# Kernel tuning notes

Hardware: AMD Instinct MI355X
Metric: run time of the kernel (lower is better)

The kernel has to match this reference:

```python
import jax, jax.numpy as jnp
import numpy as np


def setup_inputs() -> dict:
    key = jax.random.key(0)
    k1, k2, k3 = jax.random.split(key, 3)
    B, D, L = 32768, 1024, 2
    return {
        "x": jax.random.normal(k1, (B, D), dtype=jnp.float32),
        "local_angles": jax.random.normal(k2, (L, D), dtype=jnp.float32),
        "ent_angles": jax.random.normal(k3, (L, D // 2), dtype=jnp.float32),
    }


def _local_layer(out, angles):
    # Sequential chain of Givens rotations on column pairs (i, (i+1)%D).
    # Each step uses the already-updated columns, exactly like the torch loop
    # (out = out @ R.T  ==  rotate columns i and j of out).
    D = out.shape[1]
    idx = jnp.arange(D)

    def body(o, inp):
        i, theta = inp
        j = (i + 1) % D
        c, s = jnp.cos(theta), jnp.sin(theta)
        ci = jnp.take(o, i, axis=1)  # [B]
        cj = jnp.take(o, j, axis=1)  # [B]
        o = o.at[:, i].set(c * ci - s * cj)
        o = o.at[:, j].set(s * ci + c * cj)
        return o, None

    out, _ = jax.lax.scan(body, out, (idx, angles))
    return out


def _ent_layer(out, angles):
    # Entangler rotations act on disjoint pairs (2k, 2k+1) -> fully vectorized.
    B, D = out.shape
    p = out.reshape(B, D // 2, 2)
    c, s = jnp.cos(angles), jnp.sin(angles)  # [D//2]
    x0, x1 = p[..., 0], p[..., 1]
    return jnp.stack([c * x0 - s * x1, s * x0 + c * x1], axis=-1).reshape(B, D)


def reference(x, local_angles, ent_angles):
    out = x
    num_layers = local_angles.shape[0]
    for l in range(num_layers):
        out = _local_layer(out, local_angles[l])
        out = _ent_layer(out, ent_angles[l])
    return out
```

## Files before the change

kernel.cpp:

```cpp
#include <hip/hip_runtime.h>

#define D_DIM    1024
#define PER_LANE 16
#define NLAYER   2
#define NPAIR    8
#define WPB      4

__device__ __forceinline__ int swz(int c) { return c ^ ((c >> 3) & 7); }

__global__ void angles_kernel(const float* __restrict__ la,
                              const float* __restrict__ ea,
                              float* __restrict__ tab) {
    int t  = blockIdx.x * blockDim.x + threadIdx.x;
    int nt = gridDim.x * blockDim.x;
    for (int i = t; i < NLAYER * D_DIM; i += nt) {
        float s, c; sincosf(la[i], &s, &c);
        tab[i] = c; tab[2048 + i] = s;
    }
    for (int i = t; i < NLAYER * (D_DIM / 2); i += nt) {
        float s, c; sincosf(ea[i], &s, &c);
        tab[4096 + i] = c; tab[5120 + i] = s;
    }
}

__global__ __launch_bounds__(256) void qent_kernel(
        const float* __restrict__ x,
        const float* __restrict__ tab,
        float* __restrict__ out, int B)
{
    const int lane  = threadIdx.x & 63;
    const int wid   = threadIdx.x >> 6;
    const int gwave = blockIdx.x * WPB + wid;
    const int nwave = gridDim.x * WPB;

    __shared__ float4 tb[WPB][2][256];
    __shared__ float  lds_ce[NLAYER][NPAIR][64];
    __shared__ float  lds_se[NLAYER][NPAIR][64];

    for (int t = threadIdx.x; t < NLAYER * 512; t += 256) {
        int L = t >> 9, p = t & 511;
        int m = p >> 6, ln = p & 63;
        lds_ce[L][m][ln] = tab[4096 + L * 512 + ln * 8 + m];
        lds_se[L][m][ln] = tab[5120 + L * 512 + ln * 8 + m];
    }
    __syncthreads();

    float cl[NLAYER][PER_LANE], sl[NLAYER][PER_LANE];
    #pragma unroll
    for (int L = 0; L < NLAYER; ++L) {
        const float4* cp = reinterpret_cast<const float4*>(tab + L * D_DIM + lane * PER_LANE);
        const float4* sp = reinterpret_cast<const float4*>(tab + 2048 + L * D_DIM + lane * PER_LANE);
        #pragma unroll
        for (int q = 0; q < 4; ++q) {
            float4 c4 = cp[q], s4 = sp[q];
            cl[L][4*q+0] = c4.x; cl[L][4*q+1] = c4.y; cl[L][4*q+2] = c4.z; cl[L][4*q+3] = c4.w;
            sl[L][4*q+0] = s4.x; sl[L][4*q+1] = s4.y; sl[L][4*q+2] = s4.z; sl[L][4*q+3] = s4.w;
        }
    }

    const int l2 = lane ^ (lane >> 3);
    auto stage = [&](int b, int row) {
        const float* src = x + (size_t)row * D_DIM;
        #pragma unroll
        for (int q = 0; q < 4; ++q) {
            __builtin_amdgcn_global_load_lds(
                (const __attribute__((address_space(1))) void*)(src + q * 256 + l2 * 4),
                (__attribute__((address_space(3))) void*)&tb[wid][b][q * 64],
                16, 0, 0);
        }
    };

    stage(0, gwave);

    int it = 0;
    for (int row = gwave; row < B; row += nwave, ++it) {
        const int cur  = it & 1;
        const int nrow = row + nwave;

        if (nrow < B) {
            stage(cur ^ 1, nrow);
            asm volatile("s_waitcnt vmcnt(4)" ::: "memory");
        } else {
            asm volatile("s_waitcnt vmcnt(0)" ::: "memory");
        }

        float v[PER_LANE];
        #pragma unroll
        for (int r = 0; r < 4; ++r) {
            float4 t = tb[wid][cur][swz(4 * lane + r)];
            v[4*r+0] = t.x; v[4*r+1] = t.y; v[4*r+2] = t.z; v[4*r+3] = t.w;
        }

        #pragma unroll
        for (int L = 0; L < NLAYER; ++L) {
            float vnf = __shfl_down(v[0], 1);

            float A = 1.f, Bv = 0.f;
            #pragma unroll
            for (int k = 0; k < PER_LANE; ++k) {
                float vn = (k < PER_LANE - 1) ? v[k + 1] : vnf;
                Bv = sl[L][k] * Bv + cl[L][k] * vn;
                A  = sl[L][k] * A;
            }

            float Ai = A, Bi = Bv;
            #pragma unroll
            for (int dd = 1; dd < 64; dd <<= 1) {
                float Au = __shfl_up(Ai, dd);
                float Bu = __shfl_up(Bi, dd);
                if (lane >= dd) {
                    Bi = Ai * Bu + Bi;
                    Ai = Ai * Au;
                }
            }
            float Ax  = __shfl_up(Ai, 1);
            float Bx  = __shfl_up(Bi, 1);
            float v0b = __shfl(v[0], 0);
            float u   = (lane == 0) ? v[0] : (Ax * v0b + Bx);

            #pragma unroll
            for (int k = 0; k < PER_LANE - 1; ++k) {
                float vn = v[k + 1];
                float f  = cl[L][k] * u - sl[L][k] * vn;
                u        = sl[L][k] * u + cl[L][k] * vn;
                v[k] = f;
            }
            float a0   = __shfl(v[0], 0);
            float vn15 = (lane == 63) ? a0 : vnf;
            float f15  = cl[L][PER_LANE-1] * u - sl[L][PER_LANE-1] * vn15;
            float un   = sl[L][PER_LANE-1] * u + cl[L][PER_LANE-1] * vn15;
            v[PER_LANE-1] = f15;
            float f0new = __shfl(un, 63);
            if (lane == 0) v[0] = f0new;

            #pragma unroll
            for (int m = 0; m < NPAIR; ++m) {
                float cem = lds_ce[L][m][lane];
                float sem = lds_se[L][m][lane];
                float x0 = v[2*m], x1 = v[2*m+1];
                v[2*m]   = cem * x0 - sem * x1;
                v[2*m+1] = sem * x0 + cem * x1;
            }
        }

        #pragma unroll
        for (int r = 0; r < 4; ++r) {
            float4 t;
            t.x = v[4*r+0]; t.y = v[4*r+1]; t.z = v[4*r+2]; t.w = v[4*r+3];
            tb[wid][cur][swz(4 * lane + r)] = t;
        }
        float4* op = reinterpret_cast<float4*>(out + (size_t)row * D_DIM);
        #pragma unroll
        for (int q = 0; q < 4; ++q) {
            float4 t = tb[wid][cur][swz(q * 64 + lane)];
            op[q * 64 + lane] = t;
        }
    }
}

extern "C" void kernel_launch(void* const* d_in, const int* in_sizes, int n_in,
                              void* d_out, int out_size, void* d_ws, size_t ws_size,
                              hipStream_t stream) {
    const float* x  = (const float*)d_in[0];
    const float* la = (const float*)d_in[1];
    const float* ea = (const float*)d_in[2];
    float* out = (float*)d_out;
    float* tab = (float*)d_ws;
    int B = in_sizes[0] / D_DIM;

    angles_kernel<<<8, 256, 0, stream>>>(la, ea, tab);
    qent_kernel<<<1024, 256, 0, stream>>>(x, tab, out, B);
}
```

Baseline: 62.14 us.

## Use DPP row shifts for wave scan and scalar readlanes for broadcasts

Replaces the ds_bpermute-based shuffle-up prefix scan of affine (A,B) pairs with DPP row_shr and row_bcast moves, which keep the data movement inside VALU instructions and avoid LDS permute traffic. Lane-0 and lane-63 broadcasts now use readfirstlane and readlane instead of shuffles. The entangler cos/sin values are packed into float2 so each pair needs one LDS read. The wait count is relaxed to vmcnt(8) after the first iteration, but this also lets the previous row's output stores stay in flight and relies on the exact instruction ordering for correctness.

```diff
diff --git a/kernel.cpp b/kernel.cpp
--- a/kernel.cpp
+++ b/kernel.cpp
@@ -7,6 +7,12 @@
 #define WPB      4
 
 __device__ __forceinline__ int swz(int c) { return c ^ ((c >> 3) & 7); }
+
+template<int CTRL, int RMASK>
+__device__ __forceinline__ float dpp_mov(float src, float oldv) {
+    return __int_as_float(__builtin_amdgcn_update_dpp(
+        __float_as_int(oldv), __float_as_int(src), CTRL, RMASK, 0xF, false));
+}
 
 __global__ void angles_kernel(const float* __restrict__ la,
                               const float* __restrict__ ea,
@@ -34,14 +40,15 @@
     const int nwave = gridDim.x * WPB;
 
     __shared__ float4 tb[WPB][2][256];
-    __shared__ float  lds_ce[NLAYER][NPAIR][64];
-    __shared__ float  lds_se[NLAYER][NPAIR][64];
+    __shared__ float2 lds_ces[NLAYER][NPAIR][64];
 
     for (int t = threadIdx.x; t < NLAYER * 512; t += 256) {
         int L = t >> 9, p = t & 511;
         int m = p >> 6, ln = p & 63;
-        lds_ce[L][m][ln] = tab[4096 + L * 512 + ln * 8 + m];
-        lds_se[L][m][ln] = tab[5120 + L * 512 + ln * 8 + m];
+        float2 cs;
+        cs.x = tab[4096 + L * 512 + ln * 8 + m];
+        cs.y = tab[5120 + L * 512 + ln * 8 + m];
+        lds_ces[L][m][ln] = cs;
     }
     __syncthreads();
 
@@ -79,7 +86,8 @@
 
         if (nrow < B) {
             stage(cur ^ 1, nrow);
-            asm volatile("s_waitcnt vmcnt(4)" ::: "memory");
+            if (it == 0) asm volatile("s_waitcnt vmcnt(4)" ::: "memory");
+            else         asm volatile("s_waitcnt vmcnt(8)" ::: "memory");
         } else {
             asm volatile("s_waitcnt vmcnt(0)" ::: "memory");
         }
@@ -104,19 +112,24 @@
             }
 
             float Ai = A, Bi = Bv;
-            #pragma unroll
-            for (int dd = 1; dd < 64; dd <<= 1) {
-                float Au = __shfl_up(Ai, dd);
-                float Bu = __shfl_up(Bi, dd);
-                if (lane >= dd) {
-                    Bi = Ai * Bu + Bi;
-                    Ai = Ai * Au;
-                }
-            }
+            #define SCAN_STEP(CTRL, RMASK) do {                   \
+                float Au = dpp_mov<CTRL, RMASK>(Ai, 1.0f);        \
+                float Bu = dpp_mov<CTRL, RMASK>(Bi, 0.0f);        \
+                Bi = fmaf(Ai, Bu, Bi);                            \
+                Ai *= Au; } while (0)
+            SCAN_STEP(0x111, 0xF);
+            SCAN_STEP(0x112, 0xF);
+            SCAN_STEP(0x114, 0xF);
+            SCAN_STEP(0x118, 0xF);
+            SCAN_STEP(0x142, 0xA);
+            SCAN_STEP(0x143, 0xC);
+            #undef SCAN_STEP
+
             float Ax  = __shfl_up(Ai, 1);
             float Bx  = __shfl_up(Bi, 1);
-            float v0b = __shfl(v[0], 0);
-            float u   = (lane == 0) ? v[0] : (Ax * v0b + Bx);
+            float v0b = __int_as_float(
+                __builtin_amdgcn_readfirstlane(__float_as_int(v[0])));
+            float u   = (lane == 0) ? v[0] : fmaf(Ax, v0b, Bx);
 
             #pragma unroll
             for (int k = 0; k < PER_LANE - 1; ++k) {
@@ -125,21 +138,22 @@
                 u        = sl[L][k] * u + cl[L][k] * vn;
                 v[k] = f;
             }
-            float a0   = __shfl(v[0], 0);
+            float a0 = __int_as_float(
+                __builtin_amdgcn_readfirstlane(__float_as_int(v[0])));
             float vn15 = (lane == 63) ? a0 : vnf;
             float f15  = cl[L][PER_LANE-1] * u - sl[L][PER_LANE-1] * vn15;
             float un   = sl[L][PER_LANE-1] * u + cl[L][PER_LANE-1] * vn15;
             v[PER_LANE-1] = f15;
-            float f0new = __shfl(un, 63);
-            if (lane == 0) v[0] = f0new;
+            float f0new = __int_as_float(
+                __builtin_amdgcn_readlane(__float_as_int(un), 63));
+            v[0] = (lane == 0) ? f0new : v[0];
 
             #pragma unroll
             for (int m = 0; m < NPAIR; ++m) {
-                float cem = lds_ce[L][m][lane];
-                float sem = lds_se[L][m][lane];
+                float2 cs = lds_ces[L][m][lane];
                 float x0 = v[2*m], x1 = v[2*m+1];
-                v[2*m]   = cem * x0 - sem * x1;
-                v[2*m+1] = sem * x0 + cem * x1;
+                v[2*m]   = cs.x * x0 - cs.y * x1;
+                v[2*m+1] = cs.y * x0 + cs.x * x1;
             }
         }
 
```

New measurement: 57.78 us. 7.0% less time.
